# Performance work log

Hardware: AMD Instinct MI355X
Metric: run time of the kernel (lower is better)

Reference implementation:

```python
import jax, jax.numpy as jnp
import numpy as np

B, S, Ng, Np = 64, 128, 4096, 512

def setup_inputs() -> dict:
    key = jax.random.key(0)
    k = jax.random.split(key, 6)
    v = jax.random.normal(k[0], (B, S, 2), dtype=jnp.float32)
    p0 = jax.random.normal(k[1], (B, Np), dtype=jnp.float32)
    # Parameters (no biases anywhere, matching bias=False in the module)
    W_init = jax.random.normal(k[2], (Ng, Np), dtype=jnp.float32) / np.sqrt(Np)   # init_position_encoder
    W_ih = jax.random.normal(k[3], (Ng, 2), dtype=jnp.float32) / np.sqrt(Ng)      # RNN.weight_ih_l0
    W_hh = jax.random.normal(k[4], (Ng, Ng), dtype=jnp.float32) / np.sqrt(Ng)     # RNN.weight_hh_l0
    W_dec = jax.random.normal(k[5], (Np, Ng), dtype=jnp.float32) / np.sqrt(Ng)    # decoder
    return {"v": v, "p0": p0, "W_init": W_init, "W_ih": W_ih, "W_hh": W_hh, "W_dec": W_dec}

def reference(v, p0, W_init, W_ih, W_hh, W_dec):
    # h0 = Linear(Np -> Ng, no bias)(p0)
    h0 = p0 @ W_init.T                     # (B, Ng)
    # Precompute the tiny input projection for all timesteps at once
    vx = jnp.einsum('bsi,gi->sbg', v, W_ih)  # (S, B, Ng)
    def step(h, x_t):
        h = jax.nn.relu(x_t + h @ W_hh.T)  # h_t = relu(W_ih v_t + W_hh h_{t-1})
        return h, h
    _, hs = jax.lax.scan(step, h0, vx)      # hs: (S, B, Ng)
    g = jnp.transpose(hs, (1, 0, 2))        # (B, S, Ng), batch_first like torch RNN
    place_preds = g @ W_dec.T               # (B, S, Np)
    return place_preds
```

## Files before the change

kernel.cpp:

```cpp
#include <hip/hip_runtime.h>

typedef __attribute__((ext_vector_type(8))) short short8;
typedef __attribute__((ext_vector_type(4))) float f32x4;
union U16x8 { uint4 u4; short8 s8; };

__device__ inline float bf2f(unsigned short u){
  unsigned int x = ((unsigned int)u) << 16;
  float f; __builtin_memcpy(&f, &x, 4); return f;
}
__device__ inline unsigned short f2bf(float f){
  unsigned int x; __builtin_memcpy(&x, &f, 4);
  x = x + 0x7FFFu + ((x >> 16) & 1u);
  return (unsigned short)(x >> 16);
}
__device__ inline void split4(float4 f, uint2& hi, uint2& lo){
  unsigned short h0=f2bf(f.x), h1=f2bf(f.y), h2=f2bf(f.z), h3=f2bf(f.w);
  unsigned short l0=f2bf(f.x-bf2f(h0)), l1=f2bf(f.y-bf2f(h1)),
                 l2=f2bf(f.z-bf2f(h2)), l3=f2bf(f.w-bf2f(h3));
  hi = (uint2){(unsigned)h0 | ((unsigned)h1<<16), (unsigned)h2 | ((unsigned)h3<<16)};
  lo = (uint2){(unsigned)l0 | ((unsigned)l1<<16), (unsigned)l2 | ((unsigned)l3<<16)};
}
__device__ inline void split8(float4 f0, float4 f1, uint4& hi, uint4& lo){
  uint2 h0,l0,h1,l1; split4(f0,h0,l0); split4(f1,h1,l1);
  hi = (uint4){h0.x,h0.y,h1.x,h1.y};
  lo = (uint4){l0.x,l0.y,l1.x,l1.y};
}

#define MFMA16(a,b,c) __builtin_amdgcn_mfma_f32_16x16x32_bf16((a).s8,(b).s8,(c),0,0,0)

__device__ inline void st_f32_sc(float* p, float v){
  __hip_atomic_store(p, v, __ATOMIC_RELAXED, __HIP_MEMORY_SCOPE_AGENT);
}
__device__ inline void st_u32_sc(unsigned int* p, unsigned int v){
  __hip_atomic_store(p, v, __ATOMIC_RELAXED, __HIP_MEMORY_SCOPE_AGENT);
}
__device__ inline unsigned long long ld_u64_sc(const unsigned long long* p){
  return __hip_atomic_load(p, __ATOMIC_RELAXED, __HIP_MEMORY_SCOPE_AGENT);
}
__device__ inline uint4 ld_b128_sc(const unsigned short* p){
  uint4 r;
  asm volatile("global_load_dwordx4 %0, %1, off sc0 sc1"
               : "=&v"(r) : "v"(p) : "memory");
  return r;
}
__device__ inline unsigned int poll_flag(const unsigned int* p){
  unsigned int r;
  asm volatile("global_load_dword %0, %1, off sc0 sc1\n\ts_waitcnt vmcnt(0)"
               : "=&v"(r) : "v"(p) : "memory");
  return r;
}
__device__ inline void wait_vm0(){ asm volatile("s_waitcnt vmcnt(0)" ::: "memory"); }

__global__ __launch_bounds__(256)
void split_fp32(const float* __restrict__ x,
                unsigned short* __restrict__ hi,
                unsigned short* __restrict__ lo, int n4){
  int i = blockIdx.x * 256 + threadIdx.x;
  if (i >= n4) return;
  float4 v = ((const float4*)x)[i];
  ushort4 h, l;
  h.x = f2bf(v.x); l.x = f2bf(v.x - bf2f(h.x));
  h.y = f2bf(v.y); l.y = f2bf(v.y - bf2f(h.y));
  h.z = f2bf(v.z); l.z = f2bf(v.z - bf2f(h.z));
  h.w = f2bf(v.w); l.w = f2bf(v.w - bf2f(h.w));
  ((ushort4*)hi)[i] = h;
  ((ushort4*)lo)[i] = l;
}

__global__ __launch_bounds__(512, 2)
void h0_mm(const float* __restrict__ p0,
           const float* __restrict__ Wini,
           unsigned short* __restrict__ oHi,
           unsigned short* __restrict__ oLo)
{
  const int nb = blockIdx.x;
  const int tid = threadIdx.x, lane = tid & 63, wave = tid >> 6;
  const int quad = lane >> 4, l16 = lane & 15;
  const int mw = wave & 3, nw = wave >> 2;
  __shared__ __attribute__((aligned(16))) unsigned short BH[128*40];
  __shared__ __attribute__((aligned(16))) unsigned short BL[128*40];
  const int srow = tid >> 2, sk = (tid & 3) << 3;
  const float* wp = Wini + (size_t)(nb*128 + srow)*512 + sk;
  const float* ap = p0 + (size_t)(mw*16 + l16)*512 + quad*8;
  f32x4 acc[4];
  #pragma unroll
  for (int tn = 0; tn < 4; ++tn) acc[tn] = (f32x4){0.f,0.f,0.f,0.f};
  for (int kc = 0; kc < 16; ++kc){
    float4 f0 = *(const float4*)(wp + kc*32);
    float4 f1 = *(const float4*)(wp + kc*32 + 4);
    uint4 hi, lo; split8(f0, f1, hi, lo);
    __syncthreads();
    *(uint4*)&BH[srow*40 + sk] = hi;
    *(uint4*)&BL[srow*40 + sk] = lo;
    __syncthreads();
    float4 a0 = *(const float4*)(ap + kc*32);
    float4 a1 = *(const float4*)(ap + kc*32 + 4);
    uint4 ahi, alo; split8(a0, a1, ahi, alo);
    U16x8 aU, lU; aU.u4 = ahi; lU.u4 = alo;
    #pragma unroll
    for (int tn = 0; tn < 4; ++tn){
      U16x8 bh, bl;
      const int off = (nw*64 + tn*16 + l16)*40 + quad*8;
      bh.u4 = *(const uint4*)&BH[off];
      bl.u4 = *(const uint4*)&BL[off];
      acc[tn] = MFMA16(aU, bh, acc[tn]);
      acc[tn] = MFMA16(aU, bl, acc[tn]);
      acc[tn] = MFMA16(lU, bh, acc[tn]);
    }
  }
  #pragma unroll
  for (int tn = 0; tn < 4; ++tn){
    const int n = nb*128 + nw*64 + tn*16 + l16;
    #pragma unroll
    for (int r = 0; r < 4; ++r){
      const int row = mw*16 + quad*4 + r;
      const int g = n >> 3, gp = (g & ~7) | ((g & 7) ^ (row & 7));
      const int np = (gp << 3) | (n & 7);
      float val = acc[tn][r];
      unsigned short hh = f2bf(val);
      oHi[(size_t)row*4096 + np] = hh;
      oLo[(size_t)row*4096 + np] = f2bf(val - bf2f(hh));
    }
  }
}

__global__ __launch_bounds__(512, 2)
void rnn_persist(const float* __restrict__ W,
                 const float* __restrict__ v,
                 const float* __restrict__ Wih,
                 unsigned short* __restrict__ hHiA,
                 unsigned short* __restrict__ hLoA,
                 unsigned short* __restrict__ hHiB,
                 unsigned short* __restrict__ hLoB,
                 float* __restrict__ part,
                 unsigned int* __restrict__ bar,
                 unsigned short* __restrict__ G)
{
  const int bx = blockIdx.x, kb = bx & 7, nb = bx >> 3;
  const int tid = threadIdx.x, lane = tid & 63, wave = tid >> 6;
  const int quad = lane >> 4, l16 = lane & 15;
  __shared__ __attribute__((aligned(16))) unsigned short AH[64*512];
  __shared__ __attribute__((aligned(16))) unsigned short AL[64*512];

  unsigned int* partDone = bar;
  unsigned int* prodDone = bar + 1024;

  uint4 whi[16], wlo[16];
  {
    const float* wp = W + (size_t)(nb*128 + wave*16 + l16)*4096 + kb*512 + quad*8;
    #pragma unroll
    for (int c = 0; c < 16; ++c){
      float4 f0 = *(const float4*)(wp + c*32);
      float4 f1 = *(const float4*)(wp + c*32 + 4);
      split8(f0, f1, whi[c], wlo[c]);
    }
  }

  const int redM = bx >> 2;
  const int nbase = ((bx & 3) << 10) + (tid << 1);
  const int cR = kb >> 1;

  for (int s = 0; s < 128; ++s){
    const unsigned short* hH = (s & 1) ? hHiB : hHiA;
    const unsigned short* hL = (s & 1) ? hLoB : hLoA;
    unsigned short* nHi = (s & 1) ? hHiA : hHiB;
    unsigned short* nLo = (s & 1) ? hLoA : hLoB;
    float* pbuf = part + (size_t)(s & 1) * 2097152;

    if (s > 0){
      if (tid < 64){
        const unsigned int* f = prodDone + (tid*4 + cR)*4;
        while ((int)poll_flag(f) < s) __builtin_amdgcn_s_sleep(2);
      }
      __syncthreads();
    }

    {
      uint4 stg[16];
      #pragma unroll
      for (int i = 0; i < 8; ++i){
        const int flat = tid + i*512, row = flat >> 6, g = flat & 63;
        stg[i] = ld_b128_sc(hH + (size_t)row*4096 + (kb << 9) + g*8);
      }
      #pragma unroll
      for (int i = 0; i < 8; ++i){
        const int flat = tid + i*512, row = flat >> 6, g = flat & 63;
        stg[8 + i] = ld_b128_sc(hL + (size_t)row*4096 + (kb << 9) + g*8);
      }
      asm volatile("s_waitcnt vmcnt(8)" ::: "memory");
      #pragma unroll
      for (int i = 0; i < 8; ++i){
        const int flat = tid + i*512, row = flat >> 6, g = flat & 63;
        *(uint4*)&AH[row*512 + g*8] = stg[i];
      }
      asm volatile("s_waitcnt vmcnt(0)" ::: "memory");
      #pragma unroll
      for (int i = 0; i < 8; ++i){
        const int flat = tid + i*512, row = flat >> 6, g = flat & 63;
        *(uint4*)&AL[row*512 + g*8] = stg[8 + i];
      }
    }
    __syncthreads();

    f32x4 a0[4], a1[4], a2[4];
    #pragma unroll
    for (int mt = 0; mt < 4; ++mt){
      a0[mt] = (f32x4){0.f,0.f,0.f,0.f};
      a1[mt] = (f32x4){0.f,0.f,0.f,0.f};
      a2[mt] = (f32x4){0.f,0.f,0.f,0.f};
    }
    #pragma unroll
    for (int c = 0; c < 16; ++c){
      U16x8 bh, bl; bh.u4 = whi[c]; bl.u4 = wlo[c];
      #pragma unroll
      for (int mt = 0; mt < 4; ++mt){
        const int row = mt*16 + l16;
        const int gk = c*4 + quad;
        const int phys = (gk & 56) | ((gk & 7) ^ (row & 7));
        U16x8 ah, al;
        ah.u4 = *(const uint4*)&AH[row*512 + phys*8];
        al.u4 = *(const uint4*)&AL[row*512 + phys*8];
        a0[mt] = MFMA16(ah, bh, a0[mt]);
        a1[mt] = MFMA16(ah, bl, a1[mt]);
        a2[mt] = MFMA16(al, bh, a2[mt]);
      }
    }

    {
      float* pb = pbuf + (size_t)bx*8192 + wave*1024 + l16;
      #pragma unroll
      for (int mt = 0; mt < 4; ++mt)
        #pragma unroll
        for (int r = 0; r < 4; ++r)
          st_f32_sc(pb + (mt*16 + quad*4 + r)*16, a0[mt][r] + a1[mt][r] + a2[mt][r]);
    }
    wait_vm0();
    __syncthreads();
    if (tid == 0) st_u32_sc(&partDone[bx*4], (unsigned)(s + 1));

    if (tid < 64){
      const unsigned int* f = partDone + ((bx & 3)*64 + tid)*4;
      while ((int)poll_flag(f) < s + 1) __builtin_amdgcn_s_sleep(2);
    }
    __syncthreads();

    {
      float2 sum = {0.f, 0.f};
      const size_t off = (size_t)((nbase >> 4) & 7)*1024 + redM*16 + (nbase & 15);
      #pragma unroll
      for (int k2 = 0; k2 < 8; ++k2){
        unsigned long long q = ld_u64_sc((const unsigned long long*)
            (pbuf + (size_t)((nbase >> 7)*8 + k2)*8192 + off));
        float2 p; __builtin_memcpy(&p, &q, 8);
        sum.x += p.x; sum.y += p.y;
      }
      const float2 vv = *(const float2*)(v + ((size_t)redM*128 + s)*2);
      const float4 wi = *(const float4*)(Wih + (size_t)nbase*2);
      float v0 = fmaxf(sum.x + vv.x*wi.x + vv.y*wi.y, 0.f);
      float v1 = fmaxf(sum.y + vv.x*wi.z + vv.y*wi.w, 0.f);
      const unsigned short h0 = f2bf(v0), h1 = f2bf(v1);
      const unsigned short q0 = f2bf(v0 - bf2f(h0)), q1 = f2bf(v1 - bf2f(h1));
      const int g = nbase >> 3, gp = (g & ~7) | ((g & 7) ^ (redM & 7));
      const int np = (gp << 3) | (nbase & 7);
      st_u32_sc((unsigned int*)(nHi + (size_t)redM*4096 + np),
                (unsigned)h0 | ((unsigned)h1 << 16));
      st_u32_sc((unsigned int*)(nLo + (size_t)redM*4096 + np),
                (unsigned)q0 | ((unsigned)q1 << 16));
      __builtin_nontemporal_store((unsigned)h0 | ((unsigned)h1 << 16),
          (unsigned int*)(G + (size_t)s*262144 + (size_t)redM*4096 + nbase));
    }
    wait_vm0();
    __syncthreads();
    if (tid == 0) st_u32_sc(&prodDone[bx*4], (unsigned)(s + 1));
  }
}

__global__ __launch_bounds__(256, 1)
void decode_g(const unsigned short* __restrict__ G,
              const unsigned short* __restrict__ WdH,
              const unsigned short* __restrict__ WdL,
              float* __restrict__ out)
{
  const int tid = threadIdx.x, lane = tid & 63, wave = tid >> 6;
  const int quad = lane >> 4, l16 = lane & 15;
  const int wm = wave & 1, wn = wave >> 1;
  const int m0 = blockIdx.x * 128;
  const int n0 = blockIdx.y * 128;
  __shared__ __attribute__((aligned(16))) unsigned short BH[2][128*64];
  __shared__ __attribute__((aligned(16))) unsigned short BL[2][128*64];

  const unsigned short* gp[4];
  #pragma unroll
  for (int tm = 0; tm < 4; ++tm)
    gp[tm] = G + (size_t)(m0 + wm*64 + tm*16 + l16)*4096 + quad*8;

  #define LD_B(c, h4, l4) { _Pragma("unroll") \
    for (int i = 0; i < 4; ++i){ const int q = tid + i*256, row = q >> 3, gk = q & 7; \
      const size_t so = (size_t)(n0 + row)*4096 + (size_t)(c)*64 + gk*8; \
      (h4)[i] = *(const uint4*)(WdH + so); (l4)[i] = *(const uint4*)(WdL + so); } }
  #define ST_B(buf, h4, l4) { _Pragma("unroll") \
    for (int i = 0; i < 4; ++i){ const int q = tid + i*256, row = q >> 3, gk = q & 7; \
      const int phys = gk ^ (row & 7); \
      *(uint4*)&BH[buf][row*64 + phys*8] = (h4)[i]; \
      *(uint4*)&BL[buf][row*64 + phys*8] = (l4)[i]; } }
  #define LD_A(c, dst) { _Pragma("unroll") \
    for (int tm = 0; tm < 4; ++tm){ _Pragma("unroll") \
      for (int ks = 0; ks < 2; ++ks) \
        (dst)[tm][ks] = *(const uint4*)(gp[tm] + (size_t)(c)*64 + ks*32); } }

  f32x4 acc[4][4];
  #pragma unroll
  for (int a = 0; a < 4; ++a)
    #pragma unroll
    for (int b = 0; b < 4; ++b) acc[a][b] = (f32x4){0.f,0.f,0.f,0.f};

  uint4 pbh[4], pbl[4];
  uint4 ar[2][4][2];
  LD_B(0, pbh, pbl); ST_B(0, pbh, pbl);
  LD_A(0, ar[0]);
  LD_A(1, ar[1]);
  LD_B(1, pbh, pbl);
  __syncthreads();

  for (int c = 0; c < 64; ++c){
    const int cur = c & 1;
    #pragma unroll
    for (int ks = 0; ks < 2; ++ks){
      U16x8 bh[4], bl[4];
      #pragma unroll
      for (int tn = 0; tn < 4; ++tn){
        const int row = wn*64 + tn*16 + l16;
        const int gk = ks*4 + quad;
        const int phys = gk ^ (row & 7);
        bh[tn].u4 = *(const uint4*)&BH[cur][row*64 + phys*8];
        bl[tn].u4 = *(const uint4*)&BL[cur][row*64 + phys*8];
      }
      #pragma unroll
      for (int tm = 0; tm < 4; ++tm){
        U16x8 a; a.u4 = ar[cur][tm][ks];
        #pragma unroll
        for (int tn = 0; tn < 4; ++tn){
          acc[tm][tn] = MFMA16(a, bh[tn], acc[tm][tn]);
          acc[tm][tn] = MFMA16(a, bl[tn], acc[tm][tn]);
        }
      }
    }
    if (c + 2 < 64) LD_A(c+2, ar[cur]);
    if (c + 1 < 64){
      ST_B(cur ^ 1, pbh, pbl);
      if (c + 2 < 64) LD_B(c+2, pbh, pbl);
      __syncthreads();
    }
  }
  #pragma unroll
  for (int tm = 0; tm < 4; ++tm){
    #pragma unroll
    for (int tn = 0; tn < 4; ++tn){
      const int p = n0 + wn*64 + tn*16 + l16;
      #pragma unroll
      for (int r = 0; r < 4; ++r){
        const int rm = m0 + wm*64 + tm*16 + quad*4 + r;
        out[((size_t)(rm & 63)*128 + (rm >> 6))*512 + p] = acc[tm][tn][r];
      }
    }
  }
}

extern "C" void kernel_launch(void* const* d_in, const int* in_sizes, int n_in,
                              void* d_out, int out_size, void* d_ws, size_t ws_size,
                              hipStream_t stream) {
  const float* v    = (const float*)d_in[0];
  const float* p0   = (const float*)d_in[1];
  const float* Wini = (const float*)d_in[2];
  const float* Wih  = (const float*)d_in[3];
  const float* Whh  = (const float*)d_in[4];
  const float* Wdec = (const float*)d_in[5];
  float* out = (float*)d_out;
  char* wsb = (char*)d_ws;

  unsigned int*   bar  = (unsigned int*)(wsb + 0);
  unsigned short* hHiA = (unsigned short*)(wsb + 16384);
  unsigned short* hLoA = (unsigned short*)(wsb + 540672);
  unsigned short* hHiB = (unsigned short*)(wsb + 1064960);
  unsigned short* hLoB = (unsigned short*)(wsb + 1589248);
  float*          part = (float*)(wsb + 2113536);
  unsigned short* WdH  = (unsigned short*)(wsb + 18890752);
  unsigned short* WdL  = (unsigned short*)(wsb + 23085056);
  unsigned short* G    = (unsigned short*)(wsb + 27279360);

  hipMemsetAsync(bar, 0, 16384, stream);
  split_fp32<<<dim3(2048), dim3(256), 0, stream>>>(Wdec, WdH, WdL, 524288);
  h0_mm<<<dim3(32), dim3(512), 0, stream>>>(p0, Wini, hHiA, hLoA);
  rnn_persist<<<dim3(256), dim3(512), 0, stream>>>(Whh, v, Wih,
                                                   hHiA, hLoA, hHiB, hLoB,
                                                   part, bar, G);
  decode_g<<<dim3(64, 4), dim3(256), 0, stream>>>(G, WdH, WdL, out);
}
```

Before: 2.672 ms.

## Split batch rows into two halves to overlap loads and early reduction

Each recurrent step now handles the 64 batch rows in two halves of 32. The second half's hidden-state loads are issued while the first half's MFMAs run. A separate completion flag is published per half, so reducer blocks for the first 32 rows (bx<128) can start after half A finishes instead of waiting for all partials. LDS use is halved and the poll sleep is shortened, at the cost of an extra barrier, more flag traffic, and a larger flag region in the bar buffer.

```diff
diff --git a/kernel.cpp b/kernel.cpp
--- a/kernel.cpp
+++ b/kernel.cpp
@@ -139,11 +139,12 @@
   const int bx = blockIdx.x, kb = bx & 7, nb = bx >> 3;
   const int tid = threadIdx.x, lane = tid & 63, wave = tid >> 6;
   const int quad = lane >> 4, l16 = lane & 15;
-  __shared__ __attribute__((aligned(16))) unsigned short AH[64*512];
-  __shared__ __attribute__((aligned(16))) unsigned short AL[64*512];
-
-  unsigned int* partDone = bar;
-  unsigned int* prodDone = bar + 1024;
+  __shared__ __attribute__((aligned(16))) unsigned short AH[32*512];
+  __shared__ __attribute__((aligned(16))) unsigned short AL[32*512];
+
+  unsigned int* pA       = bar;
+  unsigned int* pB       = bar + 1024;
+  unsigned int* prodDone = bar + 2048;
 
   uint4 whi[16], wlo[16];
   {
@@ -159,6 +160,7 @@
   const int redM = bx >> 2;
   const int nbase = ((bx & 3) << 10) + (tid << 1);
   const int cR = kb >> 1;
+  const bool aRed = (bx < 128);
 
   for (int s = 0; s < 128; ++s){
     const unsigned short* hH = (s & 1) ? hHiB : hHiA;
@@ -170,77 +172,118 @@
     if (s > 0){
       if (tid < 64){
         const unsigned int* f = prodDone + (tid*4 + cR)*4;
-        while ((int)poll_flag(f) < s) __builtin_amdgcn_s_sleep(2);
+        while ((int)poll_flag(f) < s) __builtin_amdgcn_s_sleep(1);
       }
       __syncthreads();
     }
 
     {
-      uint4 stg[16];
-      #pragma unroll
-      for (int i = 0; i < 8; ++i){
+      uint4 stg[8];
+      #pragma unroll
+      for (int i = 0; i < 4; ++i){
         const int flat = tid + i*512, row = flat >> 6, g = flat & 63;
-        stg[i] = ld_b128_sc(hH + (size_t)row*4096 + (kb << 9) + g*8);
-      }
-      #pragma unroll
-      for (int i = 0; i < 8; ++i){
-        const int flat = tid + i*512, row = flat >> 6, g = flat & 63;
-        stg[8 + i] = ld_b128_sc(hL + (size_t)row*4096 + (kb << 9) + g*8);
-      }
-      asm volatile("s_waitcnt vmcnt(8)" ::: "memory");
-      #pragma unroll
-      for (int i = 0; i < 8; ++i){
+        stg[i]     = ld_b128_sc(hH + (size_t)row*4096 + (kb << 9) + g*8);
+        stg[4 + i] = ld_b128_sc(hL + (size_t)row*4096 + (kb << 9) + g*8);
+      }
+      wait_vm0();
+      #pragma unroll
+      for (int i = 0; i < 4; ++i){
         const int flat = tid + i*512, row = flat >> 6, g = flat & 63;
         *(uint4*)&AH[row*512 + g*8] = stg[i];
-      }
-      asm volatile("s_waitcnt vmcnt(0)" ::: "memory");
-      #pragma unroll
-      for (int i = 0; i < 8; ++i){
-        const int flat = tid + i*512, row = flat >> 6, g = flat & 63;
-        *(uint4*)&AL[row*512 + g*8] = stg[8 + i];
-      }
-    }
-    __syncthreads();
-
-    f32x4 a0[4], a1[4], a2[4];
-    #pragma unroll
-    for (int mt = 0; mt < 4; ++mt){
-      a0[mt] = (f32x4){0.f,0.f,0.f,0.f};
-      a1[mt] = (f32x4){0.f,0.f,0.f,0.f};
-      a2[mt] = (f32x4){0.f,0.f,0.f,0.f};
-    }
-    #pragma unroll
-    for (int c = 0; c < 16; ++c){
-      U16x8 bh, bl; bh.u4 = whi[c]; bl.u4 = wlo[c];
-      #pragma unroll
-      for (int mt = 0; mt < 4; ++mt){
-        const int row = mt*16 + l16;
-        const int gk = c*4 + quad;
-        const int phys = (gk & 56) | ((gk & 7) ^ (row & 7));
-        U16x8 ah, al;
-        ah.u4 = *(const uint4*)&AH[row*512 + phys*8];
-        al.u4 = *(const uint4*)&AL[row*512 + phys*8];
-        a0[mt] = MFMA16(ah, bh, a0[mt]);
-        a1[mt] = MFMA16(ah, bl, a1[mt]);
-        a2[mt] = MFMA16(al, bh, a2[mt]);
-      }
+        *(uint4*)&AL[row*512 + g*8] = stg[4 + i];
+      }
+    }
+    __syncthreads();
+
+    uint4 stgB[8];
+    #pragma unroll
+    for (int i = 0; i < 4; ++i){
+      const int flat = tid + i*512, row = 32 + (flat >> 6), g = flat & 63;
+      stgB[i]     = ld_b128_sc(hH + (size_t)row*4096 + (kb << 9) + g*8);
+      stgB[4 + i] = ld_b128_sc(hL + (size_t)row*4096 + (kb << 9) + g*8);
     }
 
     {
+      f32x4 a0[2], a1[2], a2[2];
+      #pragma unroll
+      for (int mt = 0; mt < 2; ++mt){
+        a0[mt] = (f32x4){0.f,0.f,0.f,0.f};
+        a1[mt] = (f32x4){0.f,0.f,0.f,0.f};
+        a2[mt] = (f32x4){0.f,0.f,0.f,0.f};
+      }
+      #pragma unroll
+      for (int c = 0; c < 16; ++c){
+        U16x8 bh, bl; bh.u4 = whi[c]; bl.u4 = wlo[c];
+        #pragma unroll
+        for (int mt = 0; mt < 2; ++mt){
+          const int row = mt*16 + l16;
+          const int gk = c*4 + quad;
+          const int phys = (gk & 56) | ((gk & 7) ^ (row & 7));
+          U16x8 ah, al;
+          ah.u4 = *(const uint4*)&AH[row*512 + phys*8];
+          al.u4 = *(const uint4*)&AL[row*512 + phys*8];
+          a0[mt] = MFMA16(ah, bh, a0[mt]);
+          a1[mt] = MFMA16(ah, bl, a1[mt]);
+          a2[mt] = MFMA16(al, bh, a2[mt]);
+        }
+      }
       float* pb = pbuf + (size_t)bx*8192 + wave*1024 + l16;
       #pragma unroll
-      for (int mt = 0; mt < 4; ++mt)
+      for (int mt = 0; mt < 2; ++mt)
         #pragma unroll
         for (int r = 0; r < 4; ++r)
           st_f32_sc(pb + (mt*16 + quad*4 + r)*16, a0[mt][r] + a1[mt][r] + a2[mt][r]);
     }
     wait_vm0();
     __syncthreads();
-    if (tid == 0) st_u32_sc(&partDone[bx*4], (unsigned)(s + 1));
+    if (tid == 0) st_u32_sc(&pA[bx*4], (unsigned)(s + 1));
+
+    #pragma unroll
+    for (int i = 0; i < 4; ++i){
+      const int flat = tid + i*512, row = flat >> 6, g = flat & 63;
+      *(uint4*)&AH[row*512 + g*8] = stgB[i];
+      *(uint4*)&AL[row*512 + g*8] = stgB[4 + i];
+    }
+    __syncthreads();
+
+    {
+      f32x4 a0[2], a1[2], a2[2];
+      #pragma unroll
+      for (int mt = 0; mt < 2; ++mt){
+        a0[mt] = (f32x4){0.f,0.f,0.f,0.f};
+        a1[mt] = (f32x4){0.f,0.f,0.f,0.f};
+        a2[mt] = (f32x4){0.f,0.f,0.f,0.f};
+      }
+      #pragma unroll
+      for (int c = 0; c < 16; ++c){
+        U16x8 bh, bl; bh.u4 = whi[c]; bl.u4 = wlo[c];
+        #pragma unroll
+        for (int mt = 0; mt < 2; ++mt){
+          const int row = mt*16 + l16;
+          const int gk = c*4 + quad;
+          const int phys = (gk & 56) | ((gk & 7) ^ (row & 7));
+          U16x8 ah, al;
+          ah.u4 = *(const uint4*)&AH[row*512 + phys*8];
+          al.u4 = *(const uint4*)&AL[row*512 + phys*8];
+          a0[mt] = MFMA16(ah, bh, a0[mt]);
+          a1[mt] = MFMA16(ah, bl, a1[mt]);
+          a2[mt] = MFMA16(al, bh, a2[mt]);
+        }
+      }
+      float* pb = pbuf + (size_t)bx*8192 + wave*1024 + l16;
+      #pragma unroll
+      for (int mt = 0; mt < 2; ++mt)
+        #pragma unroll
+        for (int r = 0; r < 4; ++r)
+          st_f32_sc(pb + (32 + mt*16 + quad*4 + r)*16, a0[mt][r] + a1[mt][r] + a2[mt][r]);
+    }
+    wait_vm0();
+    __syncthreads();
+    if (tid == 0) st_u32_sc(&pB[bx*4], (unsigned)(s + 1));
 
     if (tid < 64){
-      const unsigned int* f = partDone + ((bx & 3)*64 + tid)*4;
-      while ((int)poll_flag(f) < s + 1) __builtin_amdgcn_s_sleep(2);
+      const unsigned int* f = (aRed ? pA : pB) + ((bx & 3)*64 + tid)*4;
+      while ((int)poll_flag(f) < s + 1) __builtin_amdgcn_s_sleep(1);
     }
     __syncthreads();
 
```

After: 2.597 ms. 1.03x faster.
